# Performance work log

Measured on AMD Instinct MI355X. Metric: run time of the kernel, lower is better.

The kernel has to match this reference:

```python
import jax, jax.numpy as jnp
import numpy as np

ALPHA = 0.2  # LeakyReLU negative slope
NEG_INF = -9e15


def setup_inputs() -> dict:
    key = jax.random.key(0)
    k1, k2, k3, k4 = jax.random.split(key, 4)
    N, F_in, F_out = 8192, 256, 64
    h = jax.random.normal(k1, (N, F_in), dtype=jnp.float32)
    adj = jax.random.randint(k2, (N, N), 0, 2, dtype=jnp.int32)
    # xavier-uniform-style scaling for params
    W = jax.random.normal(k3, (F_in, F_out), dtype=jnp.float32) * (1.0 / np.sqrt(F_in))
    a = jax.random.normal(k4, (2 * F_out, 1), dtype=jnp.float32) * (1.0 / np.sqrt(F_out))
    return {"h": h, "adj": adj, "W": W, "a": a}


def reference(h, adj, W, a):
    # Wh: [N, F_out]
    Wh = h @ W
    F_out = W.shape[1]
    a1 = a[:F_out, 0]   # attends to source (row i)
    a2 = a[F_out:, 0]   # attends to target (row j)
    f1 = Wh @ a1        # [N]
    f2 = Wh @ a2        # [N]
    # e[i, j] = leakyrelu(Wh_i . a1 + Wh_j . a2)  == original repeat/cat math
    e = jax.nn.leaky_relu(f1[:, None] + f2[None, :], negative_slope=ALPHA)
    attention = jnp.where(adj > 0, e, NEG_INF)
    attention = jax.nn.softmax(attention, axis=1)
    # dropout omitted (eval / deterministic reference)
    h_prime = attention @ Wh  # [N, F_out]
    return jax.nn.elu(h_prime)
```

## Files before the change

kernel.cpp:

```cpp
#include <hip/hip_runtime.h>
#include <hip/hip_bf16.h>
#include <stdint.h>

#define N 8192
#define FIN 256
#define FOUT 64
#define QSPLIT 8
#define NTASK (512 * QSPLIT)
#define JLEN (N / QSPLIT)
#define NITER (JLEN / 64)

typedef __attribute__((ext_vector_type(8))) short s8v;
typedef __attribute__((ext_vector_type(4))) float f4v;

__device__ __forceinline__ uint32_t f2bf(float f) {
  uint32_t u = __float_as_uint(f);
  return (u + 0x7FFFu + ((u >> 16) & 1u)) >> 16;
}

__global__ __launch_bounds__(256) void gat_prep(
    const float* __restrict__ h, const float* __restrict__ W,
    const float* __restrict__ a,
    float* __restrict__ f1, float* __restrict__ f2,
    uint16_t* __restrict__ whT)
{
  const int c = threadIdx.x & 63;
  const int wave = threadIdx.x >> 6;
  const int i0 = blockIdx.x * 16 + wave * 4;
  float acc[4] = {0.f, 0.f, 0.f, 0.f};
  #pragma unroll 8
  for (int k = 0; k < FIN; ++k) {
    float wv = W[k * FOUT + c];
    #pragma unroll
    for (int r = 0; r < 4; ++r)
      acc[r] += h[(size_t)(i0 + r) * FIN + k] * wv;
  }
  uint32_t b0 = f2bf(acc[0]), b1 = f2bf(acc[1]), b2 = f2bf(acc[2]), b3 = f2bf(acc[3]);
  int2 pk;
  pk.x = (int)(b0 | (b1 << 16));
  pk.y = (int)(b2 | (b3 << 16));
  *(int2*)(whT + (size_t)c * N + i0) = pk;

  const float a1 = a[c], a2 = a[FOUT + c];
  #pragma unroll
  for (int r = 0; r < 4; ++r) {
    float v1 = acc[r] * a1;
    float v2 = acc[r] * a2;
    #pragma unroll
    for (int m = 32; m > 0; m >>= 1) {
      v1 += __shfl_xor(v1, m, 64);
      v2 += __shfl_xor(v2, m, 64);
    }
    if (c == 0) { f1[i0 + r] = v1; f2[i0 + r] = v2; }
  }
}

__device__ __forceinline__ s8v make_afrag_r(float f1v, int4 c0, int4 c1,
                                            float4 g0, float4 g1, float& den) {
  float e0 = f1v + g0.x; e0 = fmaxf(e0, 0.2f * e0); float w0 = (c0.x > 0) ? __expf(e0) : 0.f;
  float e1 = f1v + g0.y; e1 = fmaxf(e1, 0.2f * e1); float w1 = (c0.y > 0) ? __expf(e1) : 0.f;
  float e2 = f1v + g0.z; e2 = fmaxf(e2, 0.2f * e2); float w2 = (c0.z > 0) ? __expf(e2) : 0.f;
  float e3 = f1v + g0.w; e3 = fmaxf(e3, 0.2f * e3); float w3 = (c0.w > 0) ? __expf(e3) : 0.f;
  float e4 = f1v + g1.x; e4 = fmaxf(e4, 0.2f * e4); float w4 = (c1.x > 0) ? __expf(e4) : 0.f;
  float e5 = f1v + g1.y; e5 = fmaxf(e5, 0.2f * e5); float w5 = (c1.y > 0) ? __expf(e5) : 0.f;
  float e6 = f1v + g1.z; e6 = fmaxf(e6, 0.2f * e6); float w6 = (c1.z > 0) ? __expf(e6) : 0.f;
  float e7 = f1v + g1.w; e7 = fmaxf(e7, 0.2f * e7); float w7 = (c1.w > 0) ? __expf(e7) : 0.f;
  uint32_t b0 = f2bf(w0), b1 = f2bf(w1), b2 = f2bf(w2), b3 = f2bf(w3);
  uint32_t b4 = f2bf(w4), b5 = f2bf(w5), b6 = f2bf(w6), b7 = f2bf(w7);
  den += __uint_as_float(b0 << 16) + __uint_as_float(b1 << 16)
       + __uint_as_float(b2 << 16) + __uint_as_float(b3 << 16)
       + __uint_as_float(b4 << 16) + __uint_as_float(b5 << 16)
       + __uint_as_float(b6 << 16) + __uint_as_float(b7 << 16);
  union { s8v v; uint32_t u[4]; } r;
  r.u[0] = b0 | (b1 << 16);
  r.u[1] = b2 | (b3 << 16);
  r.u[2] = b4 | (b5 << 16);
  r.u[3] = b6 | (b7 << 16);
  return r.v;
}

__global__ __launch_bounds__(256) void gat_main2(
    const int* __restrict__ adj, const float* __restrict__ f1,
    const float* __restrict__ f2, const uint16_t* __restrict__ whT,
    float* __restrict__ pnum, float* __restrict__ pden)
{
  const int t = threadIdx.x;
  const int wave = t >> 6;
  const int lane = t & 63;
  const int task = blockIdx.x * 4 + wave;
  const int group = task / QSPLIT;
  const int quarter = task % QSPLIT;
  const int i0 = group * 16;
  const int jb = quarter * JLEN;
  const int m  = lane & 15;
  const int kg = lane >> 4;

  const float f1v = f1[i0 + m];
  const int*      ap  = adj + (size_t)(i0 + m) * N + jb + kg * 8;
  const float*    fp  = f2 + jb + kg * 8;
  const uint16_t* bp0 = whT + (size_t)m * N + jb + kg * 8;

  f4v acc0 = {0.f, 0.f, 0.f, 0.f};
  f4v acc1 = acc0, acc2 = acc0, acc3 = acc0;
  float den = 0.f;

  int4   pc0 = *(const int4*)(ap);
  int4   pc1 = *(const int4*)(ap + 4);
  int4   pc2 = *(const int4*)(ap + 32);
  int4   pc3 = *(const int4*)(ap + 36);
  float4 pg0 = *(const float4*)(fp);
  float4 pg1 = *(const float4*)(fp + 4);
  float4 pg2 = *(const float4*)(fp + 32);
  float4 pg3 = *(const float4*)(fp + 36);

  #pragma unroll 1
  for (int jc = 0; jc < NITER; ++jc) {
    const int j0 = jc * 64;
    int4 c0 = pc0, c1 = pc1, c2 = pc2, c3 = pc3;
    float4 g0 = pg0, g1 = pg1, g2 = pg2, g3 = pg3;
    if (jc + 1 < NITER) {
      const int jn = j0 + 64;
      pc0 = *(const int4*)(ap + jn);
      pc1 = *(const int4*)(ap + jn + 4);
      pc2 = *(const int4*)(ap + jn + 32);
      pc3 = *(const int4*)(ap + jn + 36);
      pg0 = *(const float4*)(fp + jn);
      pg1 = *(const float4*)(fp + jn + 4);
      pg2 = *(const float4*)(fp + jn + 32);
      pg3 = *(const float4*)(fp + jn + 36);
    }
    s8v a0 = make_afrag_r(f1v, c0, c1, g0, g1, den);
    s8v a1 = make_afrag_r(f1v, c2, c3, g2, g3, den);
    const uint16_t* bp = bp0 + j0;
    s8v b00 = *(const s8v*)(bp);
    s8v b01 = *(const s8v*)(bp + 32);
    s8v b10 = *(const s8v*)(bp + 16 * N);
    s8v b11 = *(const s8v*)(bp + 16 * N + 32);
    s8v b20 = *(const s8v*)(bp + 32 * N);
    s8v b21 = *(const s8v*)(bp + 32 * N + 32);
    s8v b30 = *(const s8v*)(bp + 48 * N);
    s8v b31 = *(const s8v*)(bp + 48 * N + 32);
    acc0 = __builtin_amdgcn_mfma_f32_16x16x32_bf16(a0, b00, acc0, 0, 0, 0);
    acc0 = __builtin_amdgcn_mfma_f32_16x16x32_bf16(a1, b01, acc0, 0, 0, 0);
    acc1 = __builtin_amdgcn_mfma_f32_16x16x32_bf16(a0, b10, acc1, 0, 0, 0);
    acc1 = __builtin_amdgcn_mfma_f32_16x16x32_bf16(a1, b11, acc1, 0, 0, 0);
    acc2 = __builtin_amdgcn_mfma_f32_16x16x32_bf16(a0, b20, acc2, 0, 0, 0);
    acc2 = __builtin_amdgcn_mfma_f32_16x16x32_bf16(a1, b21, acc2, 0, 0, 0);
    acc3 = __builtin_amdgcn_mfma_f32_16x16x32_bf16(a0, b30, acc3, 0, 0, 0);
    acc3 = __builtin_amdgcn_mfma_f32_16x16x32_bf16(a1, b31, acc3, 0, 0, 0);
  }

  den += __shfl_xor(den, 16, 64);
  den += __shfl_xor(den, 32, 64);

  float* np = pnum + (size_t)task * (16 * 64);
  #pragma unroll
  for (int r = 0; r < 4; ++r) {
    int row = kg * 4 + r;
    np[row * 64 +      m] = acc0[r];
    np[row * 64 + 16 + m] = acc1[r];
    np[row * 64 + 32 + m] = acc2[r];
    np[row * 64 + 48 + m] = acc3[r];
  }
  if (lane < 16) pden[task * 16 + m] = den;
}

__global__ __launch_bounds__(256) void gat_combine(
    const float* __restrict__ pnum, const float* __restrict__ pden,
    float* __restrict__ out)
{
  const int idx = blockIdx.x * 256 + threadIdx.x;
  const int i = idx >> 6;
  const int c = idx & 63;
  const int g = i >> 4;
  const int r = i & 15;
  const size_t base = (size_t)g * QSPLIT * 1024 + (size_t)r * 64 + c;
  float num = 0.f;
  #pragma unroll
  for (int q = 0; q < QSPLIT; ++q) num += pnum[base + (size_t)q * 1024];
  const int db = g * (QSPLIT * 16) + r;
  float den = 0.f;
  #pragma unroll
  for (int q = 0; q < QSPLIT; ++q) den += pden[db + q * 16];
  float hp = num / den;
  out[idx] = (hp > 0.f) ? hp : (__expf(hp) - 1.f);
}

extern "C" void kernel_launch(void* const* d_in, const int* in_sizes, int n_in,
                              void* d_out, int out_size, void* d_ws, size_t ws_size,
                              hipStream_t stream) {
  const float* h   = (const float*)d_in[0];
  const int*   adj = (const int*)d_in[1];
  const float* W   = (const float*)d_in[2];
  const float* a   = (const float*)d_in[3];
  float* out = (float*)d_out;

  float* f1 = (float*)d_ws;
  float* f2 = f1 + N;
  uint16_t* whT = (uint16_t*)(f2 + N);
  float* pnum = (float*)(whT + (size_t)FOUT * N);
  float* pden = pnum + (size_t)NTASK * 16 * 64;

  gat_prep<<<N / 16, 256, 0, stream>>>(h, W, a, f1, f2, whT);
  gat_main2<<<NTASK / 4, 256, 0, stream>>>(adj, f1, f2, whT, pnum, pden);
  gat_combine<<<(N * FOUT) / 256, 256, 0, stream>>>(pnum, pden, out);
}
```

Baseline: 419.2 us.

## Fuse split-K attention and combine into one block with LDS reduction

```diff
diff --git a/kernel.cpp b/kernel.cpp
--- a/kernel.cpp
+++ b/kernel.cpp
@@ -5,10 +5,8 @@
 #define N 8192
 #define FIN 256
 #define FOUT 64
-#define QSPLIT 8
-#define NTASK (512 * QSPLIT)
-#define JLEN (N / QSPLIT)
-#define NITER (JLEN / 64)
+#define WAVES 8
+#define JLEN (N / WAVES)
 
 typedef __attribute__((ext_vector_type(8))) short s8v;
 typedef __attribute__((ext_vector_type(4))) float f4v;
@@ -42,6 +40,7 @@
   *(int2*)(whT + (size_t)c * N + i0) = pk;
 
   const float a1 = a[c], a2 = a[FOUT + c];
+  const float LOG2E = 1.4426950408889634f;
   #pragma unroll
   for (int r = 0; r < 4; ++r) {
     float v1 = acc[r] * a1;
@@ -51,20 +50,20 @@
       v1 += __shfl_xor(v1, m, 64);
       v2 += __shfl_xor(v2, m, 64);
     }
-    if (c == 0) { f1[i0 + r] = v1; f2[i0 + r] = v2; }
-  }
-}
-
-__device__ __forceinline__ s8v make_afrag_r(float f1v, int4 c0, int4 c1,
-                                            float4 g0, float4 g1, float& den) {
-  float e0 = f1v + g0.x; e0 = fmaxf(e0, 0.2f * e0); float w0 = (c0.x > 0) ? __expf(e0) : 0.f;
-  float e1 = f1v + g0.y; e1 = fmaxf(e1, 0.2f * e1); float w1 = (c0.y > 0) ? __expf(e1) : 0.f;
-  float e2 = f1v + g0.z; e2 = fmaxf(e2, 0.2f * e2); float w2 = (c0.z > 0) ? __expf(e2) : 0.f;
-  float e3 = f1v + g0.w; e3 = fmaxf(e3, 0.2f * e3); float w3 = (c0.w > 0) ? __expf(e3) : 0.f;
-  float e4 = f1v + g1.x; e4 = fmaxf(e4, 0.2f * e4); float w4 = (c1.x > 0) ? __expf(e4) : 0.f;
-  float e5 = f1v + g1.y; e5 = fmaxf(e5, 0.2f * e5); float w5 = (c1.y > 0) ? __expf(e5) : 0.f;
-  float e6 = f1v + g1.z; e6 = fmaxf(e6, 0.2f * e6); float w6 = (c1.z > 0) ? __expf(e6) : 0.f;
-  float e7 = f1v + g1.w; e7 = fmaxf(e7, 0.2f * e7); float w7 = (c1.w > 0) ? __expf(e7) : 0.f;
+    if (c == 0) { f1[i0 + r] = v1 * LOG2E; f2[i0 + r] = v2 * LOG2E; }
+  }
+}
+
+__device__ __forceinline__ s8v make_afrag(float f1v, int4 c0, int4 c1,
+                                          float4 g0, float4 g1, float& den) {
+  float e0 = f1v + g0.x; e0 = fmaxf(e0, 0.2f * e0); float w0 = (c0.x > 0) ? __builtin_exp2f(e0) : 0.f;
+  float e1 = f1v + g0.y; e1 = fmaxf(e1, 0.2f * e1); float w1 = (c0.y > 0) ? __builtin_exp2f(e1) : 0.f;
+  float e2 = f1v + g0.z; e2 = fmaxf(e2, 0.2f * e2); float w2 = (c0.z > 0) ? __builtin_exp2f(e2) : 0.f;
+  float e3 = f1v + g0.w; e3 = fmaxf(e3, 0.2f * e3); float w3 = (c0.w > 0) ? __builtin_exp2f(e3) : 0.f;
+  float e4 = f1v + g1.x; e4 = fmaxf(e4, 0.2f * e4); float w4 = (c1.x > 0) ? __builtin_exp2f(e4) : 0.f;
+  float e5 = f1v + g1.y; e5 = fmaxf(e5, 0.2f * e5); float w5 = (c1.y > 0) ? __builtin_exp2f(e5) : 0.f;
+  float e6 = f1v + g1.z; e6 = fmaxf(e6, 0.2f * e6); float w6 = (c1.z > 0) ? __builtin_exp2f(e6) : 0.f;
+  float e7 = f1v + g1.w; e7 = fmaxf(e7, 0.2f * e7); float w7 = (c1.w > 0) ? __builtin_exp2f(e7) : 0.f;
   uint32_t b0 = f2bf(w0), b1 = f2bf(w1), b2 = f2bf(w2), b3 = f2bf(w3);
   uint32_t b4 = f2bf(w4), b5 = f2bf(w5), b6 = f2bf(w6), b7 = f2bf(w7);
   den += __uint_as_float(b0 << 16) + __uint_as_float(b1 << 16)
@@ -79,81 +78,94 @@
   return r.v;
 }
 
-__global__ __launch_bounds__(256) void gat_main2(
+__global__ __launch_bounds__(512, 4) void gat_fused(
     const int* __restrict__ adj, const float* __restrict__ f1,
     const float* __restrict__ f2, const uint16_t* __restrict__ whT,
-    float* __restrict__ pnum, float* __restrict__ pden)
+    float* __restrict__ out)
 {
+  __shared__ __align__(16) float lds_f2[WAVES][JLEN];
+  __shared__ __align__(16) float lds_num[WAVES][16][64];
+  __shared__ float lds_den[WAVES][16];
+
   const int t = threadIdx.x;
-  const int wave = t >> 6;
+  const int w = t >> 6;
   const int lane = t & 63;
-  const int task = blockIdx.x * 4 + wave;
-  const int group = task / QSPLIT;
-  const int quarter = task % QSPLIT;
-  const int i0 = group * 16;
-  const int jb = quarter * JLEN;
+  const int i0 = blockIdx.x * 16;
+  const int jb = w * JLEN;
   const int m  = lane & 15;
   const int kg = lane >> 4;
 
   const float f1v = f1[i0 + m];
   const int*      ap  = adj + (size_t)(i0 + m) * N + jb + kg * 8;
-  const float*    fp  = f2 + jb + kg * 8;
   const uint16_t* bp0 = whT + (size_t)m * N + jb + kg * 8;
+
+  int4 A0 = *(const int4*)(ap);
+  int4 A1 = *(const int4*)(ap + 4);
+  int4 A2 = *(const int4*)(ap + 32);
+  int4 A3 = *(const int4*)(ap + 36);
+
+  #pragma unroll
+  for (int q = 0; q < 4; ++q)
+    *(float4*)&lds_f2[w][q * 256 + lane * 4] =
+        *(const float4*)&f2[jb + q * 256 + lane * 4];
+
+  const float4* lf = (const float4*)&lds_f2[w][0];
+  const int kg2 = kg * 2;
 
   f4v acc0 = {0.f, 0.f, 0.f, 0.f};
   f4v acc1 = acc0, acc2 = acc0, acc3 = acc0;
   float den = 0.f;
 
-  int4   pc0 = *(const int4*)(ap);
-  int4   pc1 = *(const int4*)(ap + 4);
-  int4   pc2 = *(const int4*)(ap + 32);
-  int4   pc3 = *(const int4*)(ap + 36);
-  float4 pg0 = *(const float4*)(fp);
-  float4 pg1 = *(const float4*)(fp + 4);
-  float4 pg2 = *(const float4*)(fp + 32);
-  float4 pg3 = *(const float4*)(fp + 36);
+  int4 B0, B1, B2, B3;
+
+#define COMPUTE(C0, C1, C2, C3, J) do {                                     \
+    const uint16_t* bp = bp0 + (J);                                         \
+    s8v b00 = *(const s8v*)(bp);                                            \
+    s8v b01 = *(const s8v*)(bp + 32);                                       \
+    s8v b10 = *(const s8v*)(bp + 16 * N);                                   \
+    s8v b11 = *(const s8v*)(bp + 16 * N + 32);                              \
+    s8v b20 = *(const s8v*)(bp + 32 * N);                                   \
+    s8v b21 = *(const s8v*)(bp + 32 * N + 32);                              \
+    s8v b30 = *(const s8v*)(bp + 48 * N);                                   \
+    s8v b31 = *(const s8v*)(bp + 48 * N + 32);                              \
+    float4 g0 = lf[((J) >> 2) + kg2];                                       \
+    float4 g1 = lf[((J) >> 2) + kg2 + 1];                                   \
+    float4 g2 = lf[((J) >> 2) + kg2 + 8];                                   \
+    float4 g3 = lf[((J) >> 2) + kg2 + 9];                                   \
+    s8v a0 = make_afrag(f1v, C0, C1, g0, g1, den);                          \
+    s8v a1 = make_afrag(f1v, C2, C3, g2, g3, den);                          \
+    acc0 = __builtin_amdgcn_mfma_f32_16x16x32_bf16(a0, b00, acc0, 0, 0, 0); \
+    acc0 = __builtin_amdgcn_mfma_f32_16x16x32_bf16(a1, b01, acc0, 0, 0, 0); \
+    acc1 = __builtin_amdgcn_mfma_f32_16x16x32_bf16(a0, b10, acc1, 0, 0, 0); \
+    acc1 = __builtin_amdgcn_mfma_f32_16x16x32_bf16(a1, b11, acc1, 0, 0, 0); \
+    acc2 = __builtin_amdgcn_mfma_f32_16x16x32_bf16(a0, b20, acc2, 0, 0, 0); \
+    acc2 = __builtin_amdgcn_mfma_f32_16x16x32_bf16(a1, b21, acc2, 0, 0, 0); \
+    acc3 = __builtin_amdgcn_mfma_f32_16x16x32_bf16(a0, b30, acc3, 0, 0, 0); \
+    acc3 = __builtin_amdgcn_mfma_f32_16x16x32_bf16(a1, b31, acc3, 0, 0, 0); \
+  } while (0)
 
   #pragma unroll 1
-  for (int jc = 0; jc < NITER; ++jc) {
-    const int j0 = jc * 64;
-    int4 c0 = pc0, c1 = pc1, c2 = pc2, c3 = pc3;
-    float4 g0 = pg0, g1 = pg1, g2 = pg2, g3 = pg3;
-    if (jc + 1 < NITER) {
-      const int jn = j0 + 64;
-      pc0 = *(const int4*)(ap + jn);
-      pc1 = *(const int4*)(ap + jn + 4);
-      pc2 = *(const int4*)(ap + jn + 32);
-      pc3 = *(const int4*)(ap + jn + 36);
-      pg0 = *(const float4*)(fp + jn);
-      pg1 = *(const float4*)(fp + jn + 4);
-      pg2 = *(const float4*)(fp + jn + 32);
-      pg3 = *(const float4*)(fp + jn + 36);
+  for (int jc2 = 0; jc2 < 8; ++jc2) {
+    const int j0 = jc2 * 128;
+    B0 = *(const int4*)(ap + j0 + 64);
+    B1 = *(const int4*)(ap + j0 + 68);
+    B2 = *(const int4*)(ap + j0 + 96);
+    B3 = *(const int4*)(ap + j0 + 100);
+    COMPUTE(A0, A1, A2, A3, j0);
+    if (jc2 < 7) {
+      A0 = *(const int4*)(ap + j0 + 128);
+      A1 = *(const int4*)(ap + j0 + 132);
+      A2 = *(const int4*)(ap + j0 + 160);
+      A3 = *(const int4*)(ap + j0 + 164);
     }
-    s8v a0 = make_afrag_r(f1v, c0, c1, g0, g1, den);
-    s8v a1 = make_afrag_r(f1v, c2, c3, g2, g3, den);
-    const uint16_t* bp = bp0 + j0;
-    s8v b00 = *(const s8v*)(bp);
-    s8v b01 = *(const s8v*)(bp + 32);
-    s8v b10 = *(const s8v*)(bp + 16 * N);
-    s8v b11 = *(const s8v*)(bp + 16 * N + 32);
-    s8v b20 = *(const s8v*)(bp + 32 * N);
-    s8v b21 = *(const s8v*)(bp + 32 * N + 32);
-    s8v b30 = *(const s8v*)(bp + 48 * N);
-    s8v b31 = *(const s8v*)(bp + 48 * N + 32);
-    acc0 = __builtin_amdgcn_mfma_f32_16x16x32_bf16(a0, b00, acc0, 0, 0, 0);
-    acc0 = __builtin_amdgcn_mfma_f32_16x16x32_bf16(a1, b01, acc0, 0, 0, 0);
-    acc1 = __builtin_amdgcn_mfma_f32_16x16x32_bf16(a0, b10, acc1, 0, 0, 0);
-    acc1 = __builtin_amdgcn_mfma_f32_16x16x32_bf16(a1, b11, acc1, 0, 0, 0);
-    acc2 = __builtin_amdgcn_mfma_f32_16x16x32_bf16(a0, b20, acc2, 0, 0, 0);
-    acc2 = __builtin_amdgcn_mfma_f32_16x16x32_bf16(a1, b21, acc2, 0, 0, 0);
-    acc3 = __builtin_amdgcn_mfma_f32_16x16x32_bf16(a0, b30, acc3, 0, 0, 0);
-    acc3 = __builtin_amdgcn_mfma_f32_16x16x32_bf16(a1, b31, acc3, 0, 0, 0);
-  }
+    COMPUTE(B0, B1, B2, B3, j0 + 64);
+  }
+#undef COMPUTE
 
   den += __shfl_xor(den, 16, 64);
   den += __shfl_xor(den, 32, 64);
 
-  float* np = pnum + (size_t)task * (16 * 64);
+  float* np = &lds_num[w][0][0];
   #pragma unroll
   for (int r = 0; r < 4; ++r) {
     int row = kg * 4 + r;
@@ -162,28 +174,23 @@
     np[row * 64 + 32 + m] = acc2[r];
     np[row * 64 + 48 + m] = acc3[r];
   }
-  if (lane < 16) pden[task * 16 + m] = den;
-}
-
-__global__ __launch_bounds__(256) void gat_combine(
-    const float* __restrict__ pnum, const float* __restrict__ pden,
-    float* __restrict__ out)
-{
-  const int idx = blockIdx.x * 256 + threadIdx.x;
-  const int i = idx >> 6;
-  const int c = idx & 63;
-  const int g = i >> 4;
-  const int r = i & 15;
-  const size_t base = (size_t)g * QSPLIT * 1024 + (size_t)r * 64 + c;
-  float num = 0.f;
-  #pragma unroll
-  for (int q = 0; q < QSPLIT; ++q) num += pnum[base + (size_t)q * 1024];
-  const int db = g * (QSPLIT * 16) + r;
-  float den = 0.f;
-  #pragma unroll
-  for (int q = 0; q < QSPLIT; ++q) den += pden[db + q * 16];
-  float hp = num / den;
-  out[idx] = (hp > 0.f) ? hp : (__expf(hp) - 1.f);
+  if (lane < 16) lds_den[w][m] = den;
+  __syncthreads();
+
+  const int col = t & 63;
+  const int r0 = t >> 6;
+  #pragma unroll
+  for (int hh = 0; hh < 2; ++hh) {
+    const int row = r0 + hh * 8;
+    float num = 0.f, dsum = 0.f;
+    #pragma unroll
+    for (int q = 0; q < WAVES; ++q) {
+      num  += lds_num[q][row][col];
+      dsum += lds_den[q][row];
+    }
+    float hp = num / dsum;
+    out[(size_t)(i0 + row) * 64 + col] = (hp > 0.f) ? hp : (__expf(hp) - 1.f);
+  }
 }
 
 extern "C" void kernel_launch(void* const* d_in, const int* in_sizes, int n_in,
@@ -198,10 +205,7 @@
   float* f1 = (float*)d_ws;
   float* f2 = f1 + N;
   uint16_t* whT = (uint16_t*)(f2 + N);
-  float* pnum = (float*)(whT + (size_t)FOUT * N);
-  float* pden = pnum + (size_t)NTASK * 16 * 64;
 
   gat_prep<<<N / 16, 256, 0, stream>>>(h, W, a, f1, f2, whT);
-  gat_main2<<<NTASK / 4, 256, 0, stream>>>(adj, f1, f2, whT, pnum, pden);
-  gat_combine<<<(N * FOUT) / 256, 256, 0, stream>>>(pnum, pden, out);
-}
+  gat_fused<<<N / 16, 512, 0, stream>>>(adj, f1, f2, whT, out);
+}
```

Result: slower. 431.0 us (+2.8%).
